# Optimization experiments

Measured on AMD Instinct MI355X. Metric: run time of the kernel, lower is better.

The kernel has to match this reference:

```python
import jax, jax.numpy as jnp
import numpy as np

# dims: batch, history P, horizon Q, hidden D, nodes N, cells C=H*W, Z channels
B_, P_, Q_, D_, N_, C_, H_, W_, CZ = 16, 12, 12, 64, 2000, 1024, 32, 32, 2
K_DIFF = 3  # max diffusion step of DCGRUCell -> K+1 Chebyshev terms


def _mlp2(x, w1, b1, w2, b2):
    return jax.nn.relu(x @ w1 + b1) @ w2 + b2


def _st_embedding(SE, TE, sw1, sb1, sw2, sb2, tw1, tb1, tw2, tb2):
    # GMAN-style spatio-temporal embedding: SE (M,D), TE (B,P,2) ints
    se = _mlp2(SE, sw1, sb1, sw2, sb2)                                  # (M, D)
    te = jnp.concatenate([jax.nn.one_hot(TE[..., 0], 7, dtype=SE.dtype),
                          jax.nn.one_hot(TE[..., 1], 288, dtype=SE.dtype)], axis=-1)
    te = _mlp2(te, tw1, tb1, tw2, tb2)                                  # (B, P, D)
    return se[None, None] + te[:, :, None, :]                           # (B, P, M, D)


def _scaled_laplacian(adj):
    # DCRNN 'laplacian' filter: L_tilde = 2 L / lambda_max - I, lambda_max ~= 2
    A = jnp.maximum(adj, adj.T)
    d = A.sum(axis=1)
    dinv = jnp.where(d > 0, jax.lax.rsqrt(d), 0.0)
    eye = jnp.eye(A.shape[0], dtype=A.dtype)
    L = eye - (dinv[:, None] * A) * dinv[None, :]
    return L - eye


def _gconv(x, L, K):
    # Chebyshev diffusion features: x (B,N,F) -> (B,N,F*(K+1))
    xs = [x, jnp.einsum('nm,bmf->bnf', L, x)]
    for _ in range(2, K + 1):
        xs.append(2.0 * jnp.einsum('nm,bmf->bnf', L, xs[-1]) - xs[-2])
    b, n, f = x.shape
    return jnp.stack(xs, axis=-1).reshape(b, n, f * (K + 1))


def _hard_sigmoid(x):
    return jnp.clip(0.2 * x + 0.5, 0.0, 1.0)


def _conv2d(x, w):
    return jax.lax.conv_general_dilated(x, w, (1, 1), 'SAME',
        dimension_numbers=('NHWC', 'HWIO', 'NHWC'))


def _forward(X, Z, TE, adj_gg, adj_gr, gumbel_noise, se_x, se_z, movement_logits,
             stex_se_w1, stex_se_b1, stex_se_w2, stex_se_b2,
             stex_te_w1, stex_te_b1, stex_te_w2, stex_te_b2,
             stez_se_w1, stez_se_b1, stez_se_w2, stez_se_b2,
             stez_te_w1, stez_te_b1, stez_te_w2, stez_te_b2,
             fcs_z_w1, fcs_z_b1, fcs_z_w2, fcs_z_b2,
             fcs_x_in_w1, fcs_x_in_b1, fcs_x_in_w2, fcs_x_in_b2,
             mov_fc_w, mov_fc_b,
             fcs_x_out_w1, fcs_x_out_b1, fcs_x_out_w2, fcs_x_out_b2,
             convlstm_wx, convlstm_wh,
             dcgru_gate_w, dcgru_gate_b, dcgru_cand_w, dcgru_cand_b):
    B = X.shape[0]
    TEp = TE.astype(jnp.int32)[:, :P_, :]
    # --- cell branch ---
    STEZ = _st_embedding(se_z, TEp, stez_se_w1, stez_se_b1, stez_se_w2, stez_se_b2,
                         stez_te_w1, stez_te_b1, stez_te_w2, stez_te_b2)
    Zf = _mlp2(Z, fcs_z_w1, fcs_z_b1, fcs_z_w2, fcs_z_b2) + STEZ          # (B,P,C,D)
    Zg = Zf.reshape(B, P_, H_, W_, D_)
    def clstm_step(carry, x):
        h, c = carry
        gates = _conv2d(x, convlstm_wx) + _conv2d(h, convlstm_wh)         # (B,H,W,4D)
        i, f, g, o = jnp.split(gates, 4, axis=-1)
        c = _hard_sigmoid(f) * c + _hard_sigmoid(i) * jnp.tanh(g)
        h = _hard_sigmoid(o) * jnp.tanh(c)
        return (h, c), h
    hc0 = (jnp.zeros((B, H_, W_, D_), X.dtype), jnp.zeros((B, H_, W_, D_), X.dtype))
    _, hs = jax.lax.scan(clstm_step, hc0, jnp.swapaxes(Zg, 0, 1))
    Zc = jnp.swapaxes(hs, 0, 1).reshape(B, P_, C_, D_)
    # gumbel-softmax routing over cells (soft, tau=1)
    g = -jnp.log(-jnp.log(gumbel_noise + 1e-20) + 1e-20)
    mZ = jax.nn.softmax(movement_logits + g, axis=-1)                     # (C,C)
    Zc = jnp.einsum('cd,bpdk->bpck', mZ, Zc)
    Zc = jax.nn.relu(Zc @ mov_fc_w + mov_fc_b)
    ZX = jnp.einsum('nc,bpck->bpnk', adj_gr, Zc)                          # (B,P,N,D)
    # --- node branch ---
    STEX = _st_embedding(se_x, TEp, stex_se_w1, stex_se_b1, stex_se_w2, stex_se_b2,
                         stex_te_w1, stex_te_b1, stex_te_w2, stex_te_b2)
    Xf = _mlp2(X[..., None], fcs_x_in_w1, fcs_x_in_b1, fcs_x_in_w2, fcs_x_in_b2) + STEX + ZX
    L = _scaled_laplacian(adj_gg)
    def dcgru_step(h, x):
        xh = jnp.concatenate([x, h], axis=-1)                             # (B,N,2D)
        ru = jax.nn.sigmoid(_gconv(xh, L, K_DIFF) @ dcgru_gate_w + dcgru_gate_b)
        r, u = jnp.split(ru, 2, axis=-1)
        cnd = jnp.tanh(_gconv(jnp.concatenate([x, r * h], axis=-1), L, K_DIFF)
                       @ dcgru_cand_w + dcgru_cand_b)
        return u * h + (1.0 - u) * cnd, None
    h_last, _ = jax.lax.scan(dcgru_step, jnp.zeros((B, N_, D_), X.dtype),
                             jnp.swapaxes(Xf, 0, 1))                      # (B,N,D)
    Y = _mlp2(h_last, fcs_x_out_w1, fcs_x_out_b1, fcs_x_out_w2, fcs_x_out_b2)  # (B,N,Q)
    return jnp.transpose(Y, (0, 2, 1))                                    # (B,Q,N)


def setup_inputs() -> dict:
    key = jax.random.key(0)
    ks = iter(jax.random.split(key, 64))
    def rn(shape, s=0.05):
        return jax.random.normal(next(ks), shape, dtype=jnp.float32) * s
    def ru(shape):
        return jax.random.uniform(next(ks), shape, dtype=jnp.float32)
    z = lambda *s: jnp.zeros(s, jnp.float32)
    NM = K_DIFF + 1
    inp = {
        'X': rn((B_, P_, N_), 1.0),
        'Z': rn((B_, P_, C_, CZ), 1.0),
        'TE': jax.random.randint(next(ks), (B_, P_ + Q_, 2), 0, 7, dtype=jnp.int32),
        'adj_gg': ru((N_, N_)),
        'adj_gr': ru((N_, C_)) * 0.01,
        'gumbel_noise': jnp.clip(ru((C_, C_)), 1e-6, 1.0 - 1e-6),
        'se_x': rn((N_, D_)), 'se_z': rn((C_, D_)),
        'movement_logits': rn((C_, C_)),
        'stex_se_w1': rn((D_, D_)), 'stex_se_b1': z(D_), 'stex_se_w2': rn((D_, D_)), 'stex_se_b2': z(D_),
        'stex_te_w1': rn((295, D_)), 'stex_te_b1': z(D_), 'stex_te_w2': rn((D_, D_)), 'stex_te_b2': z(D_),
        'stez_se_w1': rn((D_, D_)), 'stez_se_b1': z(D_), 'stez_se_w2': rn((D_, D_)), 'stez_se_b2': z(D_),
        'stez_te_w1': rn((295, D_)), 'stez_te_b1': z(D_), 'stez_te_w2': rn((D_, D_)), 'stez_te_b2': z(D_),
        'fcs_z_w1': rn((CZ, D_)), 'fcs_z_b1': z(D_), 'fcs_z_w2': rn((D_, D_)), 'fcs_z_b2': z(D_),
        'fcs_x_in_w1': rn((1, D_)), 'fcs_x_in_b1': z(D_), 'fcs_x_in_w2': rn((D_, D_)), 'fcs_x_in_b2': z(D_),
        'mov_fc_w': rn((D_, D_)), 'mov_fc_b': z(D_),
        'fcs_x_out_w1': rn((D_, D_)), 'fcs_x_out_b1': z(D_), 'fcs_x_out_w2': rn((D_, Q_)), 'fcs_x_out_b2': z(Q_),
        'convlstm_wx': rn((3, 3, D_, 4 * D_)), 'convlstm_wh': rn((3, 3, D_, 4 * D_)),
        'dcgru_gate_w': rn((2 * D_ * NM, 2 * D_)), 'dcgru_gate_b': z(2 * D_),
        'dcgru_cand_w': rn((2 * D_ * NM, D_)), 'dcgru_cand_b': z(D_),
    }
    return inp


def reference(X, Z, TE, adj_gg, adj_gr, gumbel_noise, se_x, se_z, movement_logits,
              stex_se_w1, stex_se_b1, stex_se_w2, stex_se_b2,
              stex_te_w1, stex_te_b1, stex_te_w2, stex_te_b2,
              stez_se_w1, stez_se_b1, stez_se_w2, stez_se_b2,
              stez_te_w1, stez_te_b1, stez_te_w2, stez_te_b2,
              fcs_z_w1, fcs_z_b1, fcs_z_w2, fcs_z_b2,
              fcs_x_in_w1, fcs_x_in_b1, fcs_x_in_w2, fcs_x_in_b2,
              mov_fc_w, mov_fc_b,
              fcs_x_out_w1, fcs_x_out_b1, fcs_x_out_w2, fcs_x_out_b2,
              convlstm_wx, convlstm_wh,
              dcgru_gate_w, dcgru_gate_b, dcgru_cand_w, dcgru_cand_b):
    return _forward(X, Z, TE, adj_gg, adj_gr, gumbel_noise, se_x, se_z, movement_logits,
                    stex_se_w1, stex_se_b1, stex_se_w2, stex_se_b2,
                    stex_te_w1, stex_te_b1, stex_te_w2, stex_te_b2,
                    stez_se_w1, stez_se_b1, stez_se_w2, stez_se_b2,
                    stez_te_w1, stez_te_b1, stez_te_w2, stez_te_b2,
                    fcs_z_w1, fcs_z_b1, fcs_z_w2, fcs_z_b2,
                    fcs_x_in_w1, fcs_x_in_b1, fcs_x_in_w2, fcs_x_in_b2,
                    mov_fc_w, mov_fc_b,
                    fcs_x_out_w1, fcs_x_out_b1, fcs_x_out_w2, fcs_x_out_b2,
                    convlstm_wx, convlstm_wh,
                    dcgru_gate_w, dcgru_gate_b, dcgru_cand_w, dcgru_cand_b)
```

## Files before the change

kernel.cpp:

```cpp
#include <hip/hip_runtime.h>
#include <hip/hip_bf16.h>
#include <math.h>

typedef _Float16 fp16;
typedef _Float16 f16x8 __attribute__((ext_vector_type(8)));
typedef float f32x4 __attribute__((ext_vector_type(4)));

#define BB 16
#define PP 12
#define QQ 12
#define NN 2000
#define CC 1024

static __device__ __forceinline__ float ldf(float v) { return v; }
static __device__ __forceinline__ float ldf(fp16 v) { return (float)v; }
static __device__ __forceinline__ void stf(float* p, float v) { *p = v; }
static __device__ __forceinline__ void stf(fp16* p, float v) { *p = (fp16)v; }

static __device__ __forceinline__ void gload_lds16(const fp16* g, fp16* l) {
  __builtin_amdgcn_global_load_lds(
      (const __attribute__((address_space(1))) void*)g,
      (__attribute__((address_space(3))) void*)l, 16, 0, 0);
}

__global__ void k_f2h(fp16* __restrict__ dst, const float* __restrict__ src, long long n) {
  long long i = (long long)blockIdx.x * 256 + threadIdx.x;
  if (i < n) dst[i] = (fp16)src[i];
}

__global__ void k_wcatT(fp16* __restrict__ dst, const float* __restrict__ w39,
                        const float* __restrict__ w40) {
  int i = blockIdx.x * 256 + threadIdx.x;
  if (i >= 1152 * 256) return;
  int n = i & 255, kk = i >> 8;
  float v = (kk < 576) ? w39[kk * 256 + n] : w40[(kk - 576) * 256 + n];
  dst[(long long)n * 1152 + kk] = (fp16)v;
}

__global__ void k_gru_repackT(fp16* __restrict__ dst, const float* __restrict__ src, int O) {
  int i = blockIdx.x * 256 + threadIdx.x;
  if (i >= O * 512) return;
  int d = i >> 9;
  int kc = i & 511;
  int t = kc >> 7;
  int c = kc & 127;
  dst[i] = (fp16)src[(c * 4 + t) * O + d];
}

__global__ void k_w2T(fp16* __restrict__ dst, const float* __restrict__ src) {
  int i = blockIdx.x * 256 + threadIdx.x;
  if (i >= 4096) return;
  int d = i >> 6, k = i & 63;
  dst[i] = (fp16)src[k * 64 + d];
}

__global__ void k_dinv(const float* __restrict__ adj, float* __restrict__ dinv) {
  int row = blockIdx.x;
  float s = 0.f;
  for (int j = threadIdx.x; j < NN; j += 256)
    s += fmaxf(adj[(long long)row * NN + j], adj[(long long)j * NN + row]);
  __shared__ float red[256];
  red[threadIdx.x] = s;
  __syncthreads();
  for (int st = 128; st > 0; st >>= 1) {
    if (threadIdx.x < st) red[threadIdx.x] += red[threadIdx.x + st];
    __syncthreads();
  }
  if (threadIdx.x == 0) {
    float d = red[0];
    dinv[row] = d > 0.f ? 1.0f / sqrtf(d) : 0.f;
  }
}

__global__ void k_L(const float* __restrict__ adj, const float* __restrict__ dinv,
                    fp16* __restrict__ Lh) {
  long long i = (long long)blockIdx.x * 256 + threadIdx.x;
  if (i >= (long long)NN * NN) return;
  int r = (int)(i / NN), c = (int)(i % NN);
  float a = fmaxf(adj[(long long)r * NN + c], adj[(long long)c * NN + r]);
  Lh[(long long)r * 2048 + c] = (fp16)(-dinv[r] * a * dinv[c]);
}

__global__ void k_subdiag(fp16* __restrict__ M2) {
  int i = blockIdx.x * 256 + threadIdx.x;
  if (i >= NN) return;
  M2[(long long)i * 2048 + i] = (fp16)((float)M2[(long long)i * 2048 + i] - 1.0f);
}

__global__ void k_gumbel_softmax(const float* __restrict__ ml, const float* __restrict__ gn,
                                 fp16* __restrict__ mZ) {
  int row = blockIdx.x;
  __shared__ float buf[CC];
  __shared__ float red[256];
  int t = threadIdx.x;
  float mx = -1e30f;
  for (int j = t; j < CC; j += 256) {
    float u = gn[(long long)row * CC + j];
    float g = -logf(-logf(u + 1e-20f) + 1e-20f);
    float v = ml[(long long)row * CC + j] + g;
    buf[j] = v;
    mx = fmaxf(mx, v);
  }
  red[t] = mx;
  __syncthreads();
  for (int st = 128; st > 0; st >>= 1) {
    if (t < st) red[t] = fmaxf(red[t], red[t + st]);
    __syncthreads();
  }
  mx = red[0];
  __syncthreads();
  float s = 0.f;
  for (int j = t; j < CC; j += 256) {
    float e = expf(buf[j] - mx);
    buf[j] = e;
    s += e;
  }
  red[t] = s;
  __syncthreads();
  for (int st = 128; st > 0; st >>= 1) {
    if (t < st) red[t] += red[t + st];
    __syncthreads();
  }
  float inv = 1.0f / red[0];
  for (int j = t; j < CC; j += 256) mZ[(long long)row * CC + j] = (fp16)(buf[j] * inv);
}

__global__ void k_te(const int* __restrict__ TE, const float* __restrict__ w1,
                     const float* __restrict__ b1, float* __restrict__ tmp) {
  int i = blockIdx.x * 256 + threadIdx.x;
  if (i >= BB * PP * 64) return;
  int j = i & 63;
  int bp = i >> 6;
  int b = bp / PP, p = bp % PP;
  int te0 = TE[(b * (PP + QQ) + p) * 2 + 0];
  int te1 = TE[(b * (PP + QQ) + p) * 2 + 1];
  float v = w1[te0 * 64 + j] + w1[(7 + te1) * 64 + j] + b1[j];
  tmp[i] = fmaxf(v, 0.f);
}

__global__ void k_addb(float* __restrict__ dst, const float* __restrict__ b, int n) {
  int i = blockIdx.x * 256 + threadIdx.x;
  if (i < n) dst[i] += b[i & 63];
}

__global__ void k_zf1(const float* __restrict__ Z, const float* __restrict__ w1,
                      const float* __restrict__ b1, fp16* __restrict__ tmp) {
  long long i = (long long)blockIdx.x * 256 + threadIdx.x;
  if (i >= (long long)BB * PP * CC * 64) return;
  int j = (int)(i & 63);
  long long row = i >> 6;
  float v = Z[row * 2 + 0] * w1[j] + Z[row * 2 + 1] * w1[64 + j] + b1[j];
  tmp[i] = (fp16)fmaxf(v, 0.f);
}

__global__ void k_add_stez(fp16* __restrict__ Zf, const float* __restrict__ seZ,
                           const float* __restrict__ teZ) {
  long long i = (long long)blockIdx.x * 256 + threadIdx.x;
  if (i >= (long long)BB * PP * CC * 64) return;
  int j = (int)(i & 63);
  long long row = i >> 6;
  int c = (int)(row % CC);
  int bp = (int)(row / CC);
  Zf[i] = (fp16)((float)Zf[i] + seZ[c * 64 + j] + teZ[bp * 64 + j]);
}

template <typename TA, typename TB, typename TC>
__global__ __launch_bounds__(256) void gemm_t(
    const TA* __restrict__ A, int lda, long long sA,
    const TB* __restrict__ Bm, int ldb, long long sB,
    TC* Cm, int ldc, long long sC,
    const TC* S, long long sS,
    const float* __restrict__ bias,
    int M, int Ncols, int K, float alpha, float beta, int act) {
  int bz = blockIdx.z;
  A += (long long)bz * sA;
  Bm += (long long)bz * sB;
  Cm += (long long)bz * sC;
  if (S) S += (long long)bz * sS;
  const int row0 = blockIdx.x * 64, col0 = blockIdx.y * 64;
  __shared__ float As[16][68];
  __shared__ float Bs[16][68];
  int tid = threadIdx.x, tx = tid & 15, ty = tid >> 4;
  float acc[4][4] = {};
  for (int k0 = 0; k0 < K; k0 += 16) {
#pragma unroll
    for (int j = 0; j < 4; ++j) {
      int e = tid + 256 * j;
      int m = e >> 4, kk = e & 15;
      int gm = row0 + m;
      As[kk][m] = (gm < M) ? ldf(A[(long long)gm * lda + k0 + kk]) : 0.f;
    }
#pragma unroll
    for (int j = 0; j < 4; ++j) {
      int e = tid + 256 * j;
      int kk = e >> 6, n = e & 63;
      int gn = col0 + n;
      Bs[kk][n] = (gn < Ncols) ? ldf(Bm[(long long)(k0 + kk) * ldb + gn]) : 0.f;
    }
    __syncthreads();
#pragma unroll
    for (int kk = 0; kk < 16; ++kk) {
      float a[4], bb[4];
#pragma unroll
      for (int i = 0; i < 4; ++i) a[i] = As[kk][ty * 4 + i];
#pragma unroll
      for (int j = 0; j < 4; ++j) bb[j] = Bs[kk][tx * 4 + j];
#pragma unroll
      for (int i = 0; i < 4; ++i)
#pragma unroll
        for (int j = 0; j < 4; ++j) acc[i][j] = fmaf(a[i], bb[j], acc[i][j]);
    }
    __syncthreads();
  }
#pragma unroll
  for (int i = 0; i < 4; ++i) {
    int r = row0 + ty * 4 + i;
    if (r >= M) continue;
#pragma unroll
    for (int j = 0; j < 4; ++j) {
      int cn = col0 + tx * 4 + j;
      if (cn >= Ncols) continue;
      float v = alpha * acc[i][j];
      if (bias) v += bias[cn];
      if (S) v += beta * ldf(S[(long long)r * ldc + cn]);
      if (act == 1) v = fmaxf(v, 0.f);
      else if (act == 2) v = 1.f / (1.f + expf(-v));
      else if (act == 3) v = tanhf(v);
      stf(&Cm[(long long)r * ldc + cn], v);
    }
  }
}

template <int MT, int MODE>
__global__ __launch_bounds__(256) void mfma2(
    const fp16* __restrict__ A, int lda,
    const fp16* __restrict__ B, int ldb, long long bBatch, int bShift, long long bSlab,
    int bHi,
    fp16* __restrict__ C, int ldc, long long cBatch,
    const float* __restrict__ bias,
    fp16* __restrict__ rhOut, const fp16* __restrict__ hIn, long long xStride,
    const fp16* __restrict__ uIn, long long uStride,
    const fp16* __restrict__ xB, long long xZ,
    int M, int Ncols, int K, float alpha) {
  __shared__ fp16 As[MT][40];
  __shared__ fp16 Bs[64][40];
  const int z = blockIdx.z;
  const int gm0 = blockIdx.x * MT, n0 = blockIdx.y * 64;
  B += (long long)z * bBatch;
  C += (long long)z * cBatch;
  if (rhOut) rhOut += (long long)z * xStride;
  if (hIn) hIn += (long long)z * xStride;
  if (uIn) uIn += (long long)z * uStride;
  if (xB) xB += (long long)z * xZ;
  const int tid = threadIdx.x;
  const int lane = tid & 63, wv = tid >> 6;
  const int wr = wv >> 1, wc = wv & 1;
  const int quad = lane >> 4, ln = lane & 15;
  const unsigned bMask = (1u << bShift) - 1u;
  constexpr int WM = MT / 32;
  f32x4 acc[WM][2];
#pragma unroll
  for (int i = 0; i < WM; ++i)
#pragma unroll
    for (int j = 0; j < 2; ++j) acc[i][j] = (f32x4){0.f, 0.f, 0.f, 0.f};

  for (int k0 = 0; k0 < K; k0 += 32) {
#pragma unroll
    for (int i = 0; i < MT / 64; ++i) {
      int c = tid + 256 * i;
      int row = c >> 2, seg = c & 3;
      int gm = gm0 + row;
      int kk0 = k0 + seg * 8;
      const fp16* src = A + (long long)gm * lda + kk0;
      if (gm < M && kk0 + 8 <= K) {
        *(f16x8*)&As[row][seg * 8] = *(const f16x8*)src;
      } else {
#pragma unroll
        for (int j = 0; j < 8; ++j)
          As[row][seg * 8 + j] = (gm < M && kk0 + j < K) ? src[j] : (fp16)0.f;
      }
    }
    {
      int kk = k0 + (tid & 31);
      int ngrp = tid >> 5;
      int slab = (int)((unsigned)kk >> bShift);
      int kin = (int)((unsigned)kk & bMask);
      int col = kin + (kin >= 64 ? bHi : 0);
      int n = n0 + ngrp * 8;
      const fp16* src;
      if (xB && slab == 0 && kin < 64)
        src = xB + (long long)kin * 2048 + n;
      else
        src = B + (long long)slab * bSlab + (long long)col * ldb + n;
      if (kk < K && n + 8 <= Ncols) {
        f16x8 v = *(const f16x8*)src;
#pragma unroll
        for (int j = 0; j < 8; ++j) Bs[ngrp * 8 + j][tid & 31] = v[j];
      } else {
#pragma unroll
        for (int j = 0; j < 8; ++j)
          Bs[ngrp * 8 + j][tid & 31] = (kk < K && n + j < Ncols) ? src[j] : (fp16)0.f;
      }
    }
    __syncthreads();
    f16x8 af[WM], bf[2];
#pragma unroll
    for (int wm = 0; wm < WM; ++wm)
      af[wm] = *(const f16x8*)&As[wr * (MT / 2) + wm * 16 + ln][quad * 8];
#pragma unroll
    for (int wn = 0; wn < 2; ++wn)
      bf[wn] = *(const f16x8*)&Bs[wc * 32 + wn * 16 + ln][quad * 8];
#pragma unroll
    for (int wm = 0; wm < WM; ++wm)
#pragma unroll
      for (int wn = 0; wn < 2; ++wn)
        acc[wm][wn] =
// ... 94 lines not shown
        for (int j = 0; j < 8; ++j)
          Bs[n][seg * 8 + j] = (gn < Ncols && kk0 + j < K) ? src[j] : (fp16)0.f;
      }
    }
    __syncthreads();
    f16x8 af[WM], bf[WN];
#pragma unroll
    for (int wm = 0; wm < WM; ++wm)
      af[wm] = *(const f16x8*)&As[wr * (MT / 2) + wm * 16 + ln][quad * 8];
#pragma unroll
    for (int wn = 0; wn < WN; ++wn)
      bf[wn] = *(const f16x8*)&Bs[wc * (NT / 2) + wn * 16 + ln][quad * 8];
#pragma unroll
    for (int wm = 0; wm < WM; ++wm)
#pragma unroll
      for (int wn = 0; wn < WN; ++wn)
        acc[wm][wn] =
            __builtin_amdgcn_mfma_f32_16x16x32_f16(af[wm], bf[wn], acc[wm][wn], 0, 0, 0);
    __syncthreads();
  }
#pragma unroll
  for (int wm = 0; wm < WM; ++wm) {
#pragma unroll
    for (int wn = 0; wn < WN; ++wn) {
#pragma unroll
      for (int r = 0; r < 4; ++r) {
        int gm = gm0 + wr * (MT / 2) + wm * 16 + quad * 4 + r;
        int gn = n0 + wc * (NT / 2) + wn * 16 + ln;
        if (gm < M && gn < Ncols) {
          float v = alpha * acc[wm][wn][r];
          if (rowBias) v += rowBias[(long long)z * zRB + gm];
          if (s2T) v += s2T[(long long)gn * s2ld + gm];
          long long ci = ((long long)((unsigned)gm >> cMsh)) * cMslab +
                         (long long)(gm & cMmask) * ldc +
                         ((long long)((unsigned)gn >> cNsh)) * cNslab + (gn & cNmask);
          if (S) v += beta * (float)S[ci];
          if (act == 1) v = fmaxf(v, 0.f);
          else if (act == 2) v = 1.f / (1.f + expf(-v));
          else if (act == 3) v = tanhf(v);
          C[ci] = (fp16)v;
        }
      }
    }
  }
}

template <int MT, int NT>
__global__ __launch_bounds__(256) void mfma4(
    const fp16* __restrict__ base0, const fp16* __restrict__ base1, int rsh, int ssh,
    long long z0, long long z1, int lda,
    const fp16* __restrict__ B, int ldb, long long zB,
    fp16* __restrict__ C, int ldc, long long zC, int cMsh, long long cMslab, int cNsh,
    long long cNslab,
    const fp16* __restrict__ S, float alpha, float beta, int K) {
  __shared__ fp16 As[2][MT * 32];
  __shared__ fp16 Bs[2][NT * 32];
  const int tid = threadIdx.x;
  const int z = blockIdx.z;
  const int gm0 = blockIdx.x * MT, n0 = blockIdx.y * NT;
  B += (long long)z * zB;
  C += (long long)z * zC;
  if (S) S += (long long)z * zC;
  const unsigned cMmask = (1u << cMsh) - 1u;
  const unsigned cNmask = (1u << cNsh) - 1u;
  const int lane = tid & 63, wv = tid >> 6;
  const int wr = wv >> 1, wc = wv & 1;
  const int quad = lane >> 4, ln = lane & 15;
  constexpr int WM = MT / 32, WN = NT / 32;

  const fp16* aSrc[MT / 64];
  const fp16* bSrc[NT / 64];
#pragma unroll
  for (int i = 0; i < MT / 64; ++i) {
    int c = i * 256 + tid;
    int row = c >> 2;
    int lseg = (c & 3) ^ (row & 3);
    int gm = gm0 + row;
    unsigned b = (unsigned)gm >> rsh;
    unsigned wi = (unsigned)gm & ((1u << rsh) - 1u);
    unsigned sel = wi >> ssh;
    unsigned r = wi & ((1u << ssh) - 1u);
    const fp16* ab = sel ? (base1 + (long long)b * z1) : (base0 + (long long)b * z0);
    aSrc[i] = ab + (long long)r * lda + lseg * 8;
  }
#pragma unroll
  for (int i = 0; i < NT / 64; ++i) {
    int c = i * 256 + tid;
    int row = c >> 2;
    int lseg = (c & 3) ^ (row & 3);
    bSrc[i] = B + (long long)(n0 + row) * ldb + lseg * 8;
  }

  f32x4 acc[WM][WN];
#pragma unroll
  for (int i = 0; i < WM; ++i)
#pragma unroll
    for (int j = 0; j < WN; ++j) acc[i][j] = (f32x4){0.f, 0.f, 0.f, 0.f};

  const int sw = (quad ^ (ln & 3)) << 3;

#pragma unroll
  for (int i = 0; i < MT / 64; ++i) gload_lds16(aSrc[i], &As[0][(i * 256 + tid) * 8]);
#pragma unroll
  for (int i = 0; i < NT / 64; ++i) gload_lds16(bSrc[i], &Bs[0][(i * 256 + tid) * 8]);

  const int nk = K >> 5;
  for (int t = 0; t < nk; ++t) {
    const int buf = t & 1;
    __syncthreads();
    if (t + 1 < nk) {
      const int k1 = (t + 1) * 32;
#pragma unroll
      for (int i = 0; i < MT / 64; ++i)
        gload_lds16(aSrc[i] + k1, &As[buf ^ 1][(i * 256 + tid) * 8]);
#pragma unroll
      for (int i = 0; i < NT / 64; ++i)
        gload_lds16(bSrc[i] + k1, &Bs[buf ^ 1][(i * 256 + tid) * 8]);
    }
    f16x8 af[WM], bf[WN];
#pragma unroll
    for (int wm = 0; wm < WM; ++wm) {
      int row = wr * (MT / 2) + wm * 16 + ln;
      af[wm] = *(const f16x8*)&As[buf][row * 32 + sw];
    }
#pragma unroll
    for (int wn = 0; wn < WN; ++wn) {
      int row = wc * (NT / 2) + wn * 16 + ln;
      bf[wn] = *(const f16x8*)&Bs[buf][row * 32 + sw];
    }
#pragma unroll
    for (int wm = 0; wm < WM; ++wm)
#pragma unroll
      for (int wn = 0; wn < WN; ++wn)
        acc[wm][wn] =
            __builtin_amdgcn_mfma_f32_16x16x32_f16(af[wm], bf[wn], acc[wm][wn], 0, 0, 0);
  }
#pragma unroll
  for (int wm = 0; wm < WM; ++wm)
#pragma unroll
    for (int wn = 0; wn < WN; ++wn)
#pragma unroll
      for (int r = 0; r < 4; ++r) {
        int gm = gm0 + wr * (MT / 2) + wm * 16 + quad * 4 + r;
        int gn = n0 + wc * (NT / 2) + wn * 16 + ln;
        long long ci = ((long long)((unsigned)gm >> cMsh)) * cMslab +
                       (long long)(gm & cMmask) * ldc +
                       ((long long)((unsigned)gn >> cNsh)) * cNslab + (gn & cNmask);
        float v = alpha * acc[wm][wn][r];
        if (S) v += beta * (float)S[ci];
        C[ci] = (fp16)v;
      }
}

__global__ __launch_bounds__(256) void k_zxt(
    const fp16* __restrict__ A1, const fp16* __restrict__ B1,
    const fp16* __restrict__ A2, const fp16* __restrict__ B2,
    fp16* __restrict__ C, const float* __restrict__ teXb, const float* __restrict__ seX) {
  __shared__ fp16 As[64][40];
  __shared__ fp16 Bs[128][40];
  const int z = blockIdx.z;
  const int n0 = blockIdx.y * 128;
  A1 += (long long)z * 64 * CC;
  B2 += (long long)z * NN * 64;
  C += (long long)z * 64 * 2048;
  teXb += (long long)z * 64;
  const int tid = threadIdx.x;
  const int lane = tid & 63, wv = tid >> 6;
  const int wr = wv >> 1, wc = wv & 1;
  const int quad = lane >> 4, ln = lane & 15;
  f32x4 acc[2][4];
#pragma unroll
  for (int i = 0; i < 2; ++i)
#pragma unroll
    for (int j = 0; j < 4; ++j) acc[i][j] = (f32x4){0.f, 0.f, 0.f, 0.f};

  for (int k0 = 0; k0 < 1088; k0 += 32) {
    {
      int c = tid;
      int row = c >> 2, seg = c & 3;
      int kk0 = k0 + seg * 8;
      const fp16* src = (kk0 < 1024) ? (A1 + (long long)row * CC + kk0)
                                     : (A2 + (long long)row * 64 + (kk0 - 1024));
      *(f16x8*)&As[row][seg * 8] = *(const f16x8*)src;
    }
#pragma unroll
    for (int i = 0; i < 2; ++i) {
      int c = tid + 256 * i;
      int n = c >> 2, seg = c & 3;
      int gn = n0 + n;
      int kk0 = k0 + seg * 8;
      const fp16* src = (kk0 < 1024) ? (B1 + (long long)gn * CC + kk0)
                                     : (B2 + (long long)gn * 64 + (kk0 - 1024));
      if (gn < NN) {
        *(f16x8*)&Bs[n][seg * 8] = *(const f16x8*)src;
      } else {
#pragma unroll
        for (int j = 0; j < 8; ++j) Bs[n][seg * 8 + j] = (fp16)0.f;
      }
    }
    __syncthreads();
    f16x8 af[2], bf[4];
#pragma unroll
    for (int wm = 0; wm < 2; ++wm)
      af[wm] = *(const f16x8*)&As[wr * 32 + wm * 16 + ln][quad * 8];
#pragma unroll
    for (int wn = 0; wn < 4; ++wn)
      bf[wn] = *(const f16x8*)&Bs[wc * 64 + wn * 16 + ln][quad * 8];
#pragma unroll
    for (int wm = 0; wm < 2; ++wm)
#pragma unroll
      for (int wn = 0; wn < 4; ++wn)
        acc[wm][wn] =
            __builtin_amdgcn_mfma_f32_16x16x32_f16(af[wm], bf[wn], acc[wm][wn], 0, 0, 0);
    __syncthreads();
  }
#pragma unroll
  for (int wm = 0; wm < 2; ++wm)
#pragma unroll
    for (int wn = 0; wn < 4; ++wn)
#pragma unroll
      for (int r = 0; r < 4; ++r) {
        int gm = wr * 32 + wm * 16 + quad * 4 + r;
        int gn = n0 + wc * 64 + wn * 16 + ln;
        if (gn < NN) {
          float v = acc[wm][wn][r] + teXb[gm] + seX[(long long)gn * 64 + gm];
          C[(long long)gm * 2048 + gn] = (fp16)v;
        }
      }
}

__global__ __launch_bounds__(256) void k_conv_mfma(
    const fp16* __restrict__ Zf, const fp16* __restrict__ h,
    const fp16* __restrict__ wcatT, fp16* __restrict__ gates, int p) {
  __shared__ fp16 As[128][40];
  __shared__ fp16 Bs[64][40];
  const int gm0 = blockIdx.x * 128, n0 = blockIdx.y * 64;
  const int tid = threadIdx.x;
  const int lane = tid & 63, wv = tid >> 6;
  const int wr = wv >> 1, wc = wv & 1;
  const int quad = lane >> 4, ln = lane & 15;
  f32x4 acc[4][2];
#pragma unroll
  for (int i = 0; i < 4; ++i)
#pragma unroll
    for (int j = 0; j < 2; ++j) acc[i][j] = (f32x4){0.f, 0.f, 0.f, 0.f};

  for (int kb = 0; kb < 36; ++kb) {
    const int srcsel = kb >= 18;
    const int tap = (kb >> 1) % 9;
    const int half = kb & 1;
    const int dy = tap / 3 - 1, dx = tap % 3 - 1;
#pragma unroll
    for (int i = 0; i < 2; ++i) {
      int c = tid + 256 * i;
      int row = c >> 2, seg = c & 3;
      int m = gm0 + row;
      int b = m >> 10;
      int y = (m >> 5) & 31, x = m & 31;
      int yy = y + dy, xx = x + dx;
      bool valid = ((unsigned)yy < 32u) && ((unsigned)xx < 32u);
      f16x8 v;
      if (valid) {
        long long cell = ((long long)b << 10) + (yy << 5) + xx;
        const fp16* sp =
            srcsel ? (h + cell * 64)
                   : (Zf + ((((long long)(b * PP + p)) << 10) + (yy << 5) + xx) * 64);
        v = *(const f16x8*)(sp + half * 32 + seg * 8);
      } else {
#pragma unroll
        for (int j = 0; j < 8; ++j) v[j] = (fp16)0.f;
      }
      *(f16x8*)&As[row][seg * 8] = v;
    }
    {
      int n = tid >> 2, seg = tid & 3;
      *(f16x8*)&Bs[n][seg * 8] =
          *(const f16x8*)(wcatT + (long long)(n0 + n) * 1152 + kb * 32 + seg * 8);
    }
    __syncthreads();
    f16x8 af[4], bf[2];
#pragma unroll
    for (int wm = 0; wm < 4; ++wm)
      af[wm] = *(const f16x8*)&As[wr * 64 + wm * 16 + ln][quad * 8];
#pragma unroll
    for (int wn = 0; wn < 2; ++wn)
      bf[wn] = *(const f16x8*)&Bs[wc * 32 + wn * 16 + ln][quad * 8];
#pragma unroll
    for (int wm = 0; wm < 4; ++wm)
#pragma unroll
      for (int wn = 0; wn < 2; ++wn)
        acc[wm][wn] =
            __builtin_amdgcn_mfma_f32_16x16x32_f16(af[wm], bf[wn], acc[wm][wn], 0, 0, 0);
    __syncthreads();
  }
#pragma unroll
  for (int wm = 0; wm < 4; ++wm)
#pragma unroll
    for (int wn = 0; wn < 2; ++wn)
#pragma unroll
      for (int r = 0; r < 4; ++r) {
        int gm = gm0 + wr * 64 + wm * 16 + quad * 4 + r;
        int gn = n0 + wc * 32 + wn * 16 + ln;
        gates[(long long)gm * 256 + gn] = (fp16)acc[wm][wn][r];
      }
}

__global__ void k_clstm_update(const fp16* __restrict__ gates, float* __restrict__ c,
                               fp16* __restrict__ h, fp16* __restrict__ ZclT, int p) {
  long long i = (long long)blockIdx.x * 256 + threadIdx.x;
  if (i >= (long long)BB * CC * 64) return;
  int d = (int)(i & 63);
  long long bc = i >> 6;
  int b = (int)(bc >> 10);
  int cell = (int)(bc & 1023);
  const fp16* g = gates + (((long long)b * CC) + cell) * 256;
  float gi = (float)g[d], gf = (float)g[64 + d], gg = (float)g[128 + d],
        go = (float)g[192 + d];
  float hs_f = fminf(fmaxf(0.2f * gf + 0.5f, 0.f), 1.f);
  float hs_i = fminf(fmaxf(0.2f * gi + 0.5f, 0.f), 1.f);
  float hs_o = fminf(fmaxf(0.2f * go + 0.5f, 0.f), 1.f);
  float cv = hs_f * c[i] + hs_i * tanhf(gg);
  c[i] = cv;
  float hv = hs_o * tanhf(cv);
  h[i] = (fp16)hv;
  ZclT[(((long long)(b * PP + p)) * 64 + d) * CC + cell] = (fp16)hv;
}

__global__ void k_tmat(const float* __restrict__ X, const float* __restrict__ w1,
                       const float* __restrict__ b1, fp16* __restrict__ T, long long nrows) {
  long long i = (long long)blockIdx.x * 256 + threadIdx.x;
  if (i >= nrows * 64) return;
  int j = (int)(i & 63);
  long long row = i >> 6;
  T[i] = (fp16)fmaxf(X[row] * w1[j] + b1[j], 0.f);
}

__global__ void k_trT(const fp16* __restrict__ U0, float* __restrict__ htmp) {
  long long i = (long long)blockIdx.x * 256 + threadIdx.x;
  if (i >= (long long)BB * NN * 64) return;
  int d = (int)(i & 63);
  long long bn = i >> 6;
  int b = (int)(bn / NN);
  int n = (int)(bn % NN);
  htmp[i] = (float)U0[((long long)b * 192 + 64 + d) * 2048 + n];
}

__global__ void k_out(const float* __restrict__ Y, float* __restrict__ out) {
  int i = blockIdx.x * 256 + threadIdx.x;
  if (i >= BB * QQ * NN) return;
  int n = i % NN;
  int bq = i / NN;
  int b = bq / QQ, q = bq % QQ;
  out[i] = Y[((long long)b * NN + n) * 12 + q];
}

template <typename TA, typename TB, typename TC>
static void launch_gemm(hipStream_t stream, const TA* A, int lda, long long sA,
                        const TB* Bm, int ldb, long long sB, TC* Cm, int ldc, long long sC,
                        const TC* S, long long sS, const float* bias, int M, int Nc, int K,
                        float alpha, float beta, int act, int batch) {
  dim3 g((M + 63) / 64, (Nc + 63) / 64, batch);
  gemm_t<TA, TB, TC><<<g, dim3(256), 0, stream>>>(A, lda, sA, Bm, ldb, sB, Cm, ldc, sC, S,
                                                  sS, bias, M, Nc, K, alpha, beta, act);
}

extern "C" void kernel_launch(void* const* d_in, const int* in_sizes, int n_in,
                              void* d_out, int out_size, void* d_ws, size_t ws_size,
                              hipStream_t stream) {
  char* base = (char*)d_ws;
  size_t off = 0;
  auto alloc_bytes = [&](size_t nb) -> char* {
    char* p = base + off;
    off += (nb + 255) & ~(size_t)255;
    return p;
  };
  auto allocf = [&](size_t n) -> float* { return (float*)alloc_bytes(n * 4); };
  auto alloch = [&](size_t n) -> fp16* { return (fp16*)alloc_bytes(n * 2); };

  const float* X = (const float*)d_in[0];
  const float* Z = (const float*)d_in[1];
  const int* TE = (const int*)d_in[2];
  const float* adj_gg = (const float*)d_in[3];
  const float* adj_gr = (const float*)d_in[4];
  const float* gumbel = (const float*)d_in[5];
  const float* se_x = (const float*)d_in[6];
  const float* se_z = (const float*)d_in[7];
  const float* movement = (const float*)d_in[8];
  auto W = [&](int i) { return (const float*)d_in[i]; };

  fp16* wcatT = alloch((size_t)256 * 1152);
  fp16* gwT = alloch(128 * 512);
  fp16* cwT = alloch(64 * 512);
  fp16* w2T = alloch(64 * 64);
  fp16* w2mT = alloch(64 * 64);
  float* dinv = allocf(NN);
  fp16* LMall = alloch((size_t)6144 * 2048);
  fp16* mZh = alloch((size_t)CC * CC);
  fp16* agh2 = alloch((size_t)NN * CC);
  float* seZ = allocf(CC * 64);
  float* teZ = allocf(BB * PP * 64);
  float* seX = allocf(NN * 64);
  float* teXb = allocf(BB * PP * 64);
  float* mtmp = allocf(NN * 64);
  float* tetmp = allocf(BB * PP * 64);
  fp16* ruT = alloch((size_t)BB * 128 * NN);
  char* pool = alloc_bytes(50331648);
  fp16* Uall = (fp16*)pool;
  fp16* gates = (fp16*)pool;
  fp16* chh = (fp16*)(pool + 8388608);
  float* ccc = (float*)(pool + 12582912);
  fp16* Zmix = (fp16*)pool;
  fp16* ZmovT = (fp16*)(pool + 25165824);
  fp16* zpool = alloch((size_t)BB * PP * 64 * 2048);
  fp16* Zf = zpool;
  fp16* ZXt = zpool;
  fp16* Zc = alloch((size_t)BB * PP * CC * 64);

  if (off > ws_size) return;

  const long long uB = 192LL * 2048;
  const long long USL = 16LL * uB;
  const long long ZXB = 12LL * 64 * 2048;
  fp16* Lh = LMall;
  fp16* M2h = LMall + 2048LL * 2048;
  fp16* M3h = LMall + 4096LL * 2048;
  const int KCH = 2016;

  k_wcatT<<<dim3(1152), dim3(256), 0, stream>>>(wcatT, W(39), W(40));
  k_gru_repackT<<<dim3(256), dim3(256), 0, stream>>>(gwT, W(41), 128);
  k_gru_repackT<<<dim3(128), dim3(256), 0, stream>>>(cwT, W(43), 64);
  k_w2T<<<dim3(16), dim3(256), 0, stream>>>(w2T, W(31));
  k_w2T<<<dim3(16), dim3(256), 0, stream>>>(w2mT, W(33));
  k_dinv<<<dim3(NN), dim3(256), 0, stream>>>(adj_gg, dinv);
  hipMemsetAsync(LMall, 0, (size_t)6144 * 2048 * 2, stream);
  k_L<<<dim3((NN * NN + 255) / 256), dim3(256), 0, stream>>>(adj_gg, dinv, Lh);
  mfma4<64, 128><<<dim3(32, 16, 1), dim3(256), 0, stream>>>(
      Lh, Lh, 31, 31, 0LL, 0LL, 2048, Lh, 2048, 0LL, M2h, 2048, 0LL, 31, 0LL, 31, 0LL,
      (const fp16*)nullptr, 2.f, 0.f, KCH);
  k_subdiag<<<dim3((NN + 255) / 256), dim3(256), 0, stream>>>(M2h);
  mfma4<64, 128><<<dim3(32, 16, 1), dim3(256), 0, stream>>>(
      Lh, Lh, 31, 31, 0LL, 0LL, 2048, M2h, 2048, 0LL, M3h, 2048, 0LL, 31, 0LL, 31, 0LL,
      (const fp16*)Lh, 2.f, -1.f, KCH);
  k_gumbel_softmax<<<dim3(CC), dim3(256), 0, stream>>>(movement, gumbel, mZh);
  k_f2h<<<dim3((NN * CC + 255) / 256), dim3(256), 0, stream>>>(agh2, adj_gr,
                                                               (long long)NN * CC);

  launch_gemm(stream, se_z, 64, 0LL, W(17), 64, 0LL, mtmp, 64, 0LL, (float*)nullptr, 0LL,
              W(18), CC, 64, 64, 1.f, 0.f, 1, 1);
  launch_gemm(stream, (const float*)mtmp, 64, 0LL, W(19), 64, 0LL, seZ, 64, 0LL,
              (float*)nullptr, 0LL, W(20), CC, 64, 64, 1.f, 0.f, 0, 1);
  k_te<<<dim3((BB * PP * 64 + 255) / 256), dim3(256), 0, stream>>>(TE, W(21), W(22), tetmp);
  launch_gemm(stream, (const float*)tetmp, 64, 0LL, W(23), 64, 0LL, teZ, 64, 0LL,
              (float*)nullptr, 0LL, W(24), BB * PP, 64, 64, 1.f, 0.f, 0, 1);
  launch_gemm(stream, se_x, 64, 0LL, W(9), 64, 0LL, mtmp, 64, 0LL, (float*)nullptr, 0LL,
              W(10), NN, 64, 64, 1.f, 0.f, 1, 1);
  launch_gemm(stream, (const float*)mtmp, 64, 0LL, W(11), 64, 0LL, seX, 64, 0LL,
              (float*)nullptr, 0LL, W(12), NN, 64, 64, 1.f, 0.f, 0, 1);
  k_te<<<dim3((BB * PP * 64 + 255) / 256), dim3(256), 0, stream>>>(TE, W(13), W(14), tetmp);
  launch_gemm(stream, (const float*)tetmp, 64, 0LL, W(15), 64, 0LL, teXb, 64, 0LL,
              (float*)nullptr, 0LL, W(16), BB * PP, 64, 64, 1.f, 0.f, 0, 1);
  k_addb<<<dim3((BB * PP * 64 + 255) / 256), dim3(256), 0, stream>>>(teXb, W(32),
                                                                     BB * PP * 64);

  long long nZ = (long long)BB * PP * CC * 64;
  k_zf1<<<dim3((int)((nZ + 255) / 256)), dim3(256), 0, stream>>>(Z, W(25), W(26), Zc);
  launch_gemm(stream, (const fp16*)Zc, 64, 0LL, W(27), 64, 0LL, Zf, 64, 0LL,
              (fp16*)nullptr, 0LL, W(28), BB * PP * CC, 64, 64, 1.f, 0.f, 0, 1);
  k_add_stez<<<dim3((int)((nZ + 255) / 256)), dim3(256), 0, stream>>>(Zf, seZ, teZ);

  hipMemsetAsync(chh, 0, (size_t)BB * CC * 64 * 2, stream);
  hipMemsetAsync(ccc, 0, (size_t)BB * CC * 64 * 4, stream);
  for (int p = 0; p < PP; ++p) {
    k_conv_mfma<<<dim3(BB * CC / 128, 4), dim3(256), 0, stream>>>(Zf, chh, wcatT, gates, p);
    k_clstm_update<<<dim3((int)(((long long)BB * CC * 64 + 255) / 256)), dim3(256), 0,
                     stream>>>(gates, ccc, chh, Zc, p);
  }

  hipMemsetAsync(zpool, 0, (size_t)BB * PP * 64 * 2048 * 2, stream);

  mfma4<128, 64><<<dim3(8, 1, 192), dim3(256), 0, stream>>>(
      mZh, mZh, 31, 31, 0LL, 0LL, CC, (const fp16*)Zc, CC, (long long)64 * CC, Zmix, 64,
      (long long)CC * 64, 31, 0LL, 31, 0LL, (const fp16*)nullptr, 1.f, 0.f, CC);
  mfma3<64, 128><<<dim3(1, 8, 192), dim3(256), 0, stream>>>(
      w2mT, 64, 0LL, 31, 0LL, Zmix, 64, (long long)CC * 64, ZmovT, CC, (long long)64 * CC,
      31, 0LL, 31, 0LL, (const fp16*)nullptr, 0LL, 0.f, W(34), 0LL, nullptr, 0, 64, CC, 64,
      1.f, 1);

  fp16* Tmat = Zc;
  for (int half = 0; half < 2; ++half) {
    long long z0 = 96LL * half;
    k_tmat<<<dim3((int)((96LL * NN * 64 + 255) / 256)), dim3(256), 0, stream>>>(
        X + z0 * NN, W(29), W(30), Tmat, 96LL * NN);
    k_zxt<<<dim3(1, 16, 96), dim3(256), 0, stream>>>(
        ZmovT + z0 * 64 * CC, agh2, w2T, Tmat, ZXt + z0 * 64 * 2048, teXb + z0 * 64, seX);
  }

  fp16* U0 = Uall;
  fp16* U1 = Uall + USL;
  hipMemsetAsync(U0, 0, (size_t)USL * 2, stream);
  for (int p = 0; p < PP; ++p) {
    const fp16* xP = ZXt + (long long)p * 64 * 2048;
    mfma4<128, 128><<<dim3(16, 48, 1), dim3(256), 0, stream>>>(
        xP, U0 + 64 * 2048, 7, 6, ZXB, uB, 2048, LMall, 2048, 0LL, U1, 2048, 0LL, 7, uB,
        11, USL, (const fp16*)nullptr, 1.f, 0.f, KCH);
    mfma2<128, 1><<<dim3(1, 32, BB), dim3(256), 0, stream>>>(
        gwT, 512, Uall, 2048, uB, 7, USL, 0, ruT, NN, (long long)128 * NN, W(42),
        U0 + 128 * 2048, U0 + 64 * 2048, uB, (const fp16*)nullptr, 0LL, xP, ZXB, 128, NN,
        512, 1.f);
    mfma4<64, 128><<<dim3(16, 48, 1), dim3(256), 0, stream>>>(
        U0 + 128 * 2048, U0, 6, 31, uB, 0LL, 2048, LMall, 2048, 0LL, U1 + 128 * 2048, 2048,
        0LL, 6, uB, 11, USL, (const fp16*)nullptr, 1.f, 0.f, KCH);
    mfma2<64, 2><<<dim3(1, 32, BB), dim3(256), 0, stream>>>(
        cwT, 512, Uall, 2048, uB, 7, USL, 64, U0 + 64 * 2048, 2048, uB, W(44),
        (fp16*)nullptr, (const fp16*)nullptr, 0LL, (const fp16*)ruT, (long long)128 * NN,
        xP, ZXB, 64, NN, 512, 1.f);
  }

  float* htmp = (float*)Zc;
  float* out1 = (float*)(Zc + 5120000);
  float* out2 = (float*)(Zc + 10240000);
  k_trT<<<dim3((int)(((long long)BB * NN * 64 + 255) / 256)), dim3(256), 0, stream>>>(U0,
                                                                                      htmp);
  launch_gemm(stream, (const float*)htmp, 64, 0LL, W(35), 64, 0LL, out1, 64, 0LL,
              (float*)nullptr, 0LL, W(36), BB * NN, 64, 64, 1.f, 0.f, 1, 1);
  launch_gemm(stream, (const float*)out1, 64, 0LL, W(37), 12, 0LL, out2, 12, 0LL,
              (float*)nullptr, 0LL, W(38), BB * NN, 12, 64, 1.f, 0.f, 0, 1);
  k_out<<<dim3((BB * QQ * NN + 255) / 256), dim3(256), 0, stream>>>(out2, (float*)d_out);
}
```

Baseline: 3.314 ms.

## Double-buffer conv and ZX GEMMs with direct-to-LDS loads and padded halo layouts

Rewrites the ConvLSTM gate GEMM and the ZX GEMM to use double-buffered shared memory filled by global_load_lds with an XOR swizzle. This removes one barrier per k-step and overlaps loads with MFMA work. Zf and the hidden state move into a zero-padded 34x34 grid, so the conv kernel needs no per-tap bounds checks. The node dimension is padded to 2048 so the ZX kernel needs no row guards. In exchange the code adds extra memsets and a scatter-copy of Zf into the padded layout, and changes which pool buffers alias each other.

```diff
diff --git a/kernel.cpp b/kernel.cpp
--- a/kernel.cpp
+++ b/kernel.cpp
@@ -11,6 +11,8 @@
 #define QQ 12
 #define NN 2000
 #define CC 1024
+#define GP 34
+#define GP2 1156
 
 static __device__ __forceinline__ float ldf(float v) { return v; }
 static __device__ __forceinline__ float ldf(fp16 v) { return (float)v; }
@@ -153,15 +155,17 @@
   tmp[i] = (fp16)fmaxf(v, 0.f);
 }
 
-__global__ void k_add_stez(fp16* __restrict__ Zf, const float* __restrict__ seZ,
-                           const float* __restrict__ teZ) {
+__global__ void k_add_stez(fp16* __restrict__ dst, const fp16* __restrict__ src,
+                           const float* __restrict__ seZ, const float* __restrict__ teZ) {
   long long i = (long long)blockIdx.x * 256 + threadIdx.x;
   if (i >= (long long)BB * PP * CC * 64) return;
   int j = (int)(i & 63);
   long long row = i >> 6;
-  int c = (int)(row % CC);
-  int bp = (int)(row / CC);
-  Zf[i] = (fp16)((float)Zf[i] + seZ[c * 64 + j] + teZ[bp * 64 + j]);
+  int c = (int)(row & 1023);
+  int bp = (int)(row >> 10);
+  int pc = ((c >> 5) + 1) * GP + (c & 31) + 1;
+  dst[((long long)bp * GP2 + pc) * 64 + j] =
+      (fp16)((float)src[i] + seZ[c * 64 + j] + teZ[bp * 64 + j]);
 }
 
 template <typename TA, typename TB, typename TC>
@@ -562,67 +566,83 @@
       }
 }
 
-__global__ __launch_bounds__(256) void k_zxt(
+__global__ __launch_bounds__(256) void k_zxt4(
     const fp16* __restrict__ A1, const fp16* __restrict__ B1,
     const fp16* __restrict__ A2, const fp16* __restrict__ B2,
     fp16* __restrict__ C, const float* __restrict__ teXb, const float* __restrict__ seX) {
-  __shared__ fp16 As[64][40];
-  __shared__ fp16 Bs[128][40];
+  __shared__ fp16 As[2][64 * 32];
+  __shared__ fp16 Bs[2][128 * 32];
   const int z = blockIdx.z;
   const int n0 = blockIdx.y * 128;
-  A1 += (long long)z * 64 * CC;
-  B2 += (long long)z * NN * 64;
+  A1 += (long long)z * 64 * 1024;
+  B2 += (long long)z * 2048 * 64;
   C += (long long)z * 64 * 2048;
-  teXb += (long long)z * 64;
+  teXb += z * 64;
   const int tid = threadIdx.x;
   const int lane = tid & 63, wv = tid >> 6;
   const int wr = wv >> 1, wc = wv & 1;
   const int quad = lane >> 4, ln = lane & 15;
+
+  const fp16 *a1p, *a2p;
+  {
+    int row = tid >> 2;
+    int lseg = (tid & 3) ^ (row & 3);
+    a1p = A1 + (long long)row * 1024 + lseg * 8;
+    a2p = A2 + (long long)row * 64 + lseg * 8;
+  }
+  const fp16 *b1p[2], *b2p[2];
+#pragma unroll
+  for (int i = 0; i < 2; ++i) {
+    int c = tid + 256 * i;
+    int row = c >> 2;
+    int lseg = (c & 3) ^ (row & 3);
+    b1p[i] = B1 + (long long)(n0 + row) * 1024 + lseg * 8;
+    b2p[i] = B2 + (long long)(n0 + row) * 64 + lseg * 8;
+  }
   f32x4 acc[2][4];
 #pragma unroll
   for (int i = 0; i < 2; ++i)
 #pragma unroll
     for (int j = 0; j < 4; ++j) acc[i][j] = (f32x4){0.f, 0.f, 0.f, 0.f};
 
-  for (int k0 = 0; k0 < 1088; k0 += 32) {
-    {
-      int c = tid;
-      int row = c >> 2, seg = c & 3;
-      int kk0 = k0 + seg * 8;
-      const fp16* src = (kk0 < 1024) ? (A1 + (long long)row * CC + kk0)
-                                     : (A2 + (long long)row * 64 + (kk0 - 1024));
-      *(f16x8*)&As[row][seg * 8] = *(const f16x8*)src;
-    }
-#pragma unroll
-    for (int i = 0; i < 2; ++i) {
-      int c = tid + 256 * i;
-      int n = c >> 2, seg = c & 3;
-      int gn = n0 + n;
-      int kk0 = k0 + seg * 8;
-      const fp16* src = (kk0 < 1024) ? (B1 + (long long)gn * CC + kk0)
-                                     : (B2 + (long long)gn * 64 + (kk0 - 1024));
-      if (gn < NN) {
-        *(f16x8*)&Bs[n][seg * 8] = *(const f16x8*)src;
-      } else {
-#pragma unroll
-        for (int j = 0; j < 8; ++j) Bs[n][seg * 8 + j] = (fp16)0.f;
-      }
-    }
-    __syncthreads();
+  auto stage = [&](int t, int buf) {
+    if (t < 32) {
+      int k1 = t * 32;
+      gload_lds16(a1p + k1, &As[buf][tid * 8]);
+#pragma unroll
+      for (int i = 0; i < 2; ++i)
+        gload_lds16(b1p[i] + k1, &Bs[buf][(i * 256 + tid) * 8]);
+    } else {
+      int k1 = (t - 32) * 32;
+      gload_lds16(a2p + k1, &As[buf][tid * 8]);
+#pragma unroll
+      for (int i = 0; i < 2; ++i)
+        gload_lds16(b2p[i] + k1, &Bs[buf][(i * 256 + tid) * 8]);
+    }
+  };
+  stage(0, 0);
+  const int sw = (quad ^ (ln & 3)) << 3;
+  for (int t = 0; t < 34; ++t) {
+    const int buf = t & 1;
+    __syncthreads();
+    if (t + 1 < 34) stage(t + 1, buf ^ 1);
     f16x8 af[2], bf[4];
 #pragma unroll
-    for (int wm = 0; wm < 2; ++wm)
-      af[wm] = *(const f16x8*)&As[wr * 32 + wm * 16 + ln][quad * 8];
-#pragma unroll
-    for (int wn = 0; wn < 4; ++wn)
-      bf[wn] = *(const f16x8*)&Bs[wc * 64 + wn * 16 + ln][quad * 8];
+    for (int wm = 0; wm < 2; ++wm) {
+      int row = wr * 32 + wm * 16 + ln;
+      af[wm] = *(const f16x8*)&As[buf][row * 32 + sw];
+    }
+#pragma unroll
+    for (int wn = 0; wn < 4; ++wn) {
+      int row = wc * 64 + wn * 16 + ln;
+      bf[wn] = *(const f16x8*)&Bs[buf][row * 32 + sw];
+    }
 #pragma unroll
     for (int wm = 0; wm < 2; ++wm)
 #pragma unroll
       for (int wn = 0; wn < 4; ++wn)
         acc[wm][wn] =
             __builtin_amdgcn_mfma_f32_16x16x32_f16(af[wm], bf[wn], acc[wm][wn], 0, 0, 0);
-    __syncthreads();
   }
 #pragma unroll
   for (int wm = 0; wm < 2; ++wm)
@@ -632,76 +652,81 @@
       for (int r = 0; r < 4; ++r) {
         int gm = wr * 32 + wm * 16 + quad * 4 + r;
         int gn = n0 + wc * 64 + wn * 16 + ln;
-        if (gn < NN) {
-          float v = acc[wm][wn][r] + teXb[gm] + seX[(long long)gn * 64 + gm];
-          C[(long long)gm * 2048 + gn] = (fp16)v;
-        }
+        float v = (gn < NN) ? (acc[wm][wn][r] + teXb[gm] + seX[(long long)gn * 64 + gm])
+                            : 0.f;
+        C[(long long)gm * 2048 + gn] = (fp16)v;
       }
 }
 
-__global__ __launch_bounds__(256) void k_conv_mfma(
-    const fp16* __restrict__ Zf, const fp16* __restrict__ h,
+__global__ __launch_bounds__(256) void k_conv4(
+    const fp16* __restrict__ Zfp, const fp16* __restrict__ hp,
     const fp16* __restrict__ wcatT, fp16* __restrict__ gates, int p) {
-  __shared__ fp16 As[128][40];
-  __shared__ fp16 Bs[64][40];
+  __shared__ fp16 As[2][128 * 32];
+  __shared__ fp16 Bs[2][64 * 32];
   const int gm0 = blockIdx.x * 128, n0 = blockIdx.y * 64;
   const int tid = threadIdx.x;
   const int lane = tid & 63, wv = tid >> 6;
   const int wr = wv >> 1, wc = wv & 1;
   const int quad = lane >> 4, ln = lane & 15;
+
+  long long aZ[2], aH[2];
+#pragma unroll
+  for (int i = 0; i < 2; ++i) {
+    int c = tid + 256 * i;
+    int row = c >> 2;
+    int lseg = (c & 3) ^ (row & 3);
+    int m = gm0 + row;
+    int b = m >> 10, y = (m >> 5) & 31, x = m & 31;
+    int pc = (y + 1) * GP + (x + 1);
+    aZ[i] = ((long long)(b * PP + p) * GP2 + pc) * 64 + lseg * 8;
+    aH[i] = ((long long)b * GP2 + pc) * 64 + lseg * 8;
+  }
+  const fp16* bBase;
+  {
+    int row = tid >> 2;
+    int lseg = (tid & 3) ^ (row & 3);
+    bBase = wcatT + (long long)(n0 + row) * 1152 + lseg * 8;
+  }
   f32x4 acc[4][2];
 #pragma unroll
   for (int i = 0; i < 4; ++i)
 #pragma unroll
     for (int j = 0; j < 2; ++j) acc[i][j] = (f32x4){0.f, 0.f, 0.f, 0.f};
 
-  for (int kb = 0; kb < 36; ++kb) {
-    const int srcsel = kb >= 18;
-    const int tap = (kb >> 1) % 9;
-    const int half = kb & 1;
-    const int dy = tap / 3 - 1, dx = tap % 3 - 1;
+  auto stage = [&](int t, int buf) {
+    int tap = (t >> 1) % 9, half = t & 1;
+    int srcsel = t >= 18;
+    int off = ((tap / 3 - 1) * GP + (tap % 3 - 1)) * 64 + half * 32;
 #pragma unroll
     for (int i = 0; i < 2; ++i) {
-      int c = tid + 256 * i;
-      int row = c >> 2, seg = c & 3;
-      int m = gm0 + row;
-      int b = m >> 10;
-      int y = (m >> 5) & 31, x = m & 31;
-      int yy = y + dy, xx = x + dx;
-      bool valid = ((unsigned)yy < 32u) && ((unsigned)xx < 32u);
-      f16x8 v;
-      if (valid) {
-        long long cell = ((long long)b << 10) + (yy << 5) + xx;
-        const fp16* sp =
-            srcsel ? (h + cell * 64)
-                   : (Zf + ((((long long)(b * PP + p)) << 10) + (yy << 5) + xx) * 64);
-        v = *(const f16x8*)(sp + half * 32 + seg * 8);
-      } else {
-#pragma unroll
-        for (int j = 0; j < 8; ++j) v[j] = (fp16)0.f;
-      }
-      *(f16x8*)&As[row][seg * 8] = v;
-    }
-    {
-      int n = tid >> 2, seg = tid & 3;
-      *(f16x8*)&Bs[n][seg * 8] =
-          *(const f16x8*)(wcatT + (long long)(n0 + n) * 1152 + kb * 32 + seg * 8);
-    }
-    __syncthreads();
+      const fp16* src = srcsel ? (hp + aH[i] + off) : (Zfp + aZ[i] + off);
+      gload_lds16(src, &As[buf][(i * 256 + tid) * 8]);
+    }
+    gload_lds16(bBase + t * 32, &Bs[buf][tid * 8]);
+  };
+  stage(0, 0);
+  const int sw = (quad ^ (ln & 3)) << 3;
+  for (int t = 0; t < 36; ++t) {
+    const int buf = t & 1;
+    __syncthreads();
+    if (t + 1 < 36) stage(t + 1, buf ^ 1);
     f16x8 af[4], bf[2];
 #pragma unroll
-    for (int wm = 0; wm < 4; ++wm)
-      af[wm] = *(const f16x8*)&As[wr * 64 + wm * 16 + ln][quad * 8];
-#pragma unroll
-    for (int wn = 0; wn < 2; ++wn)
-      bf[wn] = *(const f16x8*)&Bs[wc * 32 + wn * 16 + ln][quad * 8];
+    for (int wm = 0; wm < 4; ++wm) {
+      int row = wr * 64 + wm * 16 + ln;
+      af[wm] = *(const f16x8*)&As[buf][row * 32 + sw];
+    }
+#pragma unroll
+    for (int wn = 0; wn < 2; ++wn) {
+      int row = wc * 32 + wn * 16 + ln;
+      bf[wn] = *(const f16x8*)&Bs[buf][row * 32 + sw];
+    }
 #pragma unroll
     for (int wm = 0; wm < 4; ++wm)
 #pragma unroll
       for (int wn = 0; wn < 2; ++wn)
         acc[wm][wn] =
             __builtin_amdgcn_mfma_f32_16x16x32_f16(af[wm], bf[wn], acc[wm][wn], 0, 0, 0);
-    __syncthreads();
   }
 #pragma unroll
   for (int wm = 0; wm < 4; ++wm)
@@ -732,7 +757,8 @@
   float cv = hs_f * c[i] + hs_i * tanhf(gg);
   c[i] = cv;
   float hv = hs_o * tanhf(cv);
-  h[i] = (fp16)hv;
+  int pc = ((cell >> 5) + 1) * GP + (cell & 31) + 1;
+  h[((long long)b * GP2 + pc) * 64 + d] = (fp16)hv;
   ZclT[(((long long)(b * PP + p)) * 64 + d) * CC + cell] = (fp16)hv;
 }
 
@@ -742,7 +768,9 @@
   if (i >= nrows * 64) return;
   int j = (int)(i & 63);
   long long row = i >> 6;
-  T[i] = (fp16)fmaxf(X[row] * w1[j] + b1[j], 0.f);
+  int z = (int)(row / NN);
+  int n = (int)(row - (long long)z * NN);
+  T[(((long long)z * 2048) + n) * 64 + j] = (fp16)fmaxf(X[row] * w1[j] + b1[j], 0.f);
 }
 
 __global__ void k_trT(const fp16* __restrict__ U0, float* __restrict__ htmp) {
@@ -806,7 +834,7 @@
   float* dinv = allocf(NN);
   fp16* LMall = alloch((size_t)6144 * 2048);
   fp16* mZh = alloch((size_t)CC * CC);
-  fp16* agh2 = alloch((size_t)NN * CC);
+  fp16* agh2 = alloch((size_t)2048 * CC);
   float* seZ = allocf(CC * 64);
   float* teZ = allocf(BB * PP * 64);
   float* seX = allocf(NN * 64);
@@ -816,13 +844,14 @@
   fp16* ruT = alloch((size_t)BB * 128 * NN);
   char* pool = alloc_bytes(50331648);
   fp16* Uall = (fp16*)pool;
+  fp16* Zftmp = (fp16*)pool;
   fp16* gates = (fp16*)pool;
   fp16* chh = (fp16*)(pool + 8388608);
   float* ccc = (float*)(pool + 12582912);
   fp16* Zmix = (fp16*)pool;
   fp16* ZmovT = (fp16*)(pool + 25165824);
   fp16* zpool = alloch((size_t)BB * PP * 64 * 2048);
-  fp16* Zf = zpool;
+  fp16* Zfp = zpool;
   fp16* ZXt = zpool;
   fp16* Zc = alloch((size_t)BB * PP * CC * 64);
 
@@ -854,6 +883,7 @@
   k_gumbel_softmax<<<dim3(CC), dim3(256), 0, stream>>>(movement, gumbel, mZh);
   k_f2h<<<dim3((NN * CC + 255) / 256), dim3(256), 0, stream>>>(agh2, adj_gr,
                                                                (long long)NN * CC);
+  hipMemsetAsync(agh2 + (size_t)NN * CC, 0, (size_t)(2048 - NN) * CC * 2, stream);
 
   launch_gemm(stream, se_z, 64, 0LL, W(17), 64, 0LL, mtmp, 64, 0LL, (float*)nullptr, 0LL,
               W(18), CC, 64, 64, 1.f, 0.f, 1, 1);
@@ -874,19 +904,18 @@
 
   long long nZ = (long long)BB * PP * CC * 64;
   k_zf1<<<dim3((int)((nZ + 255) / 256)), dim3(256), 0, stream>>>(Z, W(25), W(26), Zc);
-  launch_gemm(stream, (const fp16*)Zc, 64, 0LL, W(27), 64, 0LL, Zf, 64, 0LL,
+  launch_gemm(stream, (const fp16*)Zc, 64, 0LL, W(27), 64, 0LL, Zftmp, 64, 0LL,
               (fp16*)nullptr, 0LL, W(28), BB * PP * CC, 64, 64, 1.f, 0.f, 0, 1);
-  k_add_stez<<<dim3((int)((nZ + 255) / 256)), dim3(256), 0, stream>>>(Zf, seZ, teZ);
-
-  hipMemsetAsync(chh, 0, (size_t)BB * CC * 64 * 2, stream);
+  hipMemsetAsync(zpool, 0, (size_t)BB * PP * GP2 * 64 * 2, stream);
+  k_add_stez<<<dim3((int)((nZ + 255) / 256)), dim3(256), 0, stream>>>(Zfp, Zftmp, seZ, teZ);
+
+  hipMemsetAsync(chh, 0, (size_t)BB * GP2 * 64 * 2, stream);
   hipMemsetAsync(ccc, 0, (size_t)BB * CC * 64 * 4, stream);
   for (int p = 0; p < PP; ++p) {
-    k_conv_mfma<<<dim3(BB * CC / 128, 4), dim3(256), 0, stream>>>(Zf, chh, wcatT, gates, p);
+    k_conv4<<<dim3(BB * CC / 128, 4), dim3(256), 0, stream>>>(Zfp, chh, wcatT, gates, p);
     k_clstm_update<<<dim3((int)(((long long)BB * CC * 64 + 255) / 256)), dim3(256), 0,
                      stream>>>(gates, ccc, chh, Zc, p);
   }
-
-  hipMemsetAsync(zpool, 0, (size_t)BB * PP * 64 * 2048 * 2, stream);
 
   mfma4<128, 64><<<dim3(8, 1, 192), dim3(256), 0, stream>>>(
       mZh, mZh, 31, 31, 0LL, 0LL, CC, (const fp16*)Zc, CC, (long long)64 * CC, Zmix, 64,
@@ -901,7 +930,7 @@
     long long z0 = 96LL * half;
     k_tmat<<<dim3((int)((96LL * NN * 64 + 255) / 256)), dim3(256), 0, stream>>>(
         X + z0 * NN, W(29), W(30), Tmat, 96LL * NN);
-    k_zxt<<<dim3(1, 16, 96), dim3(256), 0, stream>>>(
+    k_zxt4<<<dim3(1, 16, 96), dim3(256), 0, stream>>>(
         ZmovT + z0 * 64 * CC, agh2, w2T, Tmat, ZXt + z0 * 64 * 2048, teXb + z0 * 64, seX);
   }
 
```

Result: faster. 3.220 ms (-2.8%).
